# Optimization experiments

Hardware: AMD Instinct MI355X
Metric: run time of the kernel (lower is better)

## Reference

```python
import jax, jax.numpy as jnp
import numpy as np

B = 16          # batch (number of point clouds)
N = 16384       # total points across batch
H = 512         # hidden_size
E = 64          # traj_embed_size
T = 8           # max_traj_len
EB = 72         # euler_bins = 360 // 5
OUT = EB * 3 + 2  # action_mlp output: 216 rot logits + open + stop = 218
TEMP = 1.0


def setup_inputs() -> dict:
    key = jax.random.key(0)
    ks = jax.random.split(key, 8)
    rng = np.random.default_rng(0)
    # ragged segment sizes, each >= 256, summing exactly to N
    counts = rng.multinomial(N - B * 256, np.ones(B) / B) + 256
    s = 0.02
    return {
        "point_embeds": jax.random.normal(ks[0], (N, H), jnp.float32),
        "coords": jax.random.normal(ks[1], (N, 3), jnp.float32),
        "traj_emb": jax.random.normal(ks[2], (T, E), jnp.float32) * s,
        "hm_w1": jax.random.normal(ks[3], (H + E, H), jnp.float32) * s,
        "hm_b1": jnp.zeros((H,), jnp.float32),
        "hm_w2": jax.random.normal(ks[4], (H, 4), jnp.float32) * s,
        "hm_b2": jnp.zeros((4,), jnp.float32),
        "act_w1": jax.random.normal(ks[5], (H + E, H), jnp.float32) * s,
        "act_b1": jnp.zeros((H,), jnp.float32),
        "act_w2": jax.random.normal(ks[6], (H, OUT), jnp.float32) * s,
        "act_b2": jnp.zeros((OUT,), jnp.float32),
        "npoints_in_batch": jnp.asarray(counts, jnp.int32),
    }


def _lrelu(x):
    return jnp.where(x >= 0, x, 0.02 * x)


def reference(point_embeds, coords, traj_emb, hm_w1, hm_b1, hm_w2, hm_b2,
              act_w1, act_b1, act_w2, act_b2, npoints_in_batch):
    n = point_embeds.shape[0]
    # segment id per point (replaces torch.split over ragged batch)
    seg = jnp.repeat(jnp.arange(B), npoints_in_batch, total_repeat_length=n)  # (N,)

    # expand with trajectory-step embedding: (N, T, H+E)
    pe = jnp.concatenate([
        jnp.broadcast_to(point_embeds[:, None, :], (n, T, H)),
        jnp.broadcast_to(traj_emb[None, :, :], (n, T, E)),
    ], axis=-1)

    # heatmap MLP: (N, T, 4) = [heatmap logit, delta xyz]
    hm = _lrelu(pe @ hm_w1 + hm_b1) @ hm_w2 + hm_b2
    logits = hm[..., 0]                                # (N, T)

    # per-segment stable softmax over points
    m = jax.ops.segment_max(logits, seg, num_segments=B)          # (B, T)
    e = jnp.exp((logits - m[seg]) / TEMP)                         # (N, T)
    z = jax.ops.segment_sum(e, seg, num_segments=B)               # (B, T)
    h = e / z[seg]                                                # (N, T)

    new_coords = coords[:, None, :] + hm[..., 1:]                 # (N, T, 3)
    xt = jax.ops.segment_sum(h[..., None] * new_coords, seg, num_segments=B)  # (B, T, 3)

    # reduce == 'max': per-segment max pooling of point embeds
    pc = jax.ops.segment_max(pe, seg, num_segments=B)             # (B, T, H+E)
    ae = _lrelu(pc @ act_w1 + act_b1) @ act_w2 + act_b2           # (B, T, 218)

    xr = ae[..., :EB * 3].reshape(B, T, EB, 3)  # euler_disc logits
    xo = ae[..., -2]
    xstop = ae[..., -1]
    return (xt, xr, xo, xstop)
```

## Files before the change

### kernel.cpp

```cpp
#include <hip/hip_runtime.h>
#include <math.h>

typedef unsigned short u16;
typedef unsigned int u32;

#define NPTS 16384
#define HID  512
#define TT   8
#define TE   64
#define NB   16
#define OUTC 218

typedef short s16x8 __attribute__((ext_vector_type(8)));
typedef float f32x4 __attribute__((ext_vector_type(4)));

__device__ __forceinline__ float bf2f(u16 u) {
  return __uint_as_float(((u32)u) << 16);
}
__device__ __forceinline__ u16 f2bf(float f) {
  u32 x = __float_as_uint(f);
  x += 0x7fffu + ((x >> 16) & 1u);
  return (u16)(x >> 16);
}
__device__ __forceinline__ float lrelu(float h) { return fmaxf(h, 0.02f * h); }

__device__ __forceinline__ float rd(const void* p, size_t i, bool f32) {
  return f32 ? ((const float*)p)[i] : bf2f(((const u16*)p)[i]);
}
__device__ __forceinline__ void wr(void* p, size_t i, bool f32, float v) {
  if (f32) ((float*)p)[i] = v;
  else ((u16*)p)[i] = f2bf(v);
}

__device__ __forceinline__ void split_bf16(float x, u16& hi, u16& lo) {
  const u32 xu = __float_as_uint(x);
  hi = (u16)(xu >> 16);
  const float rem = x - __uint_as_float(xu & 0xffff0000u);
  lo = f2bf(rem);
}

__global__ __launch_bounds__(256) void sniff_kernel(const u16* __restrict__ pe,
                                                    int* __restrict__ flag) {
  __shared__ int s;
  const int tid = threadIdx.x;
  if (tid == 0) s = 0;
  __syncthreads();
  int c = 0;
  for (int i = tid; i < 8192; i += 256) {
    const u16 v = pe[i];
    if ((v & 0x7F80u) == 0x7F80u) c = 1;
  }
  if (c) s = 1;
  __syncthreads();
  if (tid == 0) flag[0] = s;
}

__global__ __launch_bounds__(256) void prep_conv_kernel(
    const void* __restrict__ hm_w1, const void* __restrict__ hm_b1,
    const void* __restrict__ traj, const void* __restrict__ hm_w2,
    const void* __restrict__ hm_b2, const void* __restrict__ aw1,
    const void* __restrict__ ab1, const void* __restrict__ pe,
    const int* __restrict__ npts, float* __restrict__ vprime,
    float* __restrict__ w2f, float* __restrict__ b2f,
    float* __restrict__ avp, u16* __restrict__ Bth, u16* __restrict__ Btl,
    float* __restrict__ partial, const int* __restrict__ flag) {
  const bool f32 = flag[0] != 0;
  const int tid = threadIdx.x, blk = blockIdx.x;
  if (blk < 8) {
    const int t = blk;
    for (int j = tid; j < 512; j += 256) {
      float acc = rd(hm_b1, j, f32);
      for (int e = 0; e < 64; ++e)
        acc = fmaf(rd(traj, t * 64 + e, f32),
                   rd(hm_w1, (size_t)(512 + e) * 512 + j, f32), acc);
      vprime[t * 512 + j] = acc;
    }
  } else if (blk < 16) {
    const int t = blk - 8;
    for (int j = tid; j < 512; j += 256) {
      float acc = rd(ab1, j, f32);
      for (int e = 0; e < 64; ++e)
        acc = fmaf(rd(traj, t * 64 + e, f32),
                   rd(aw1, (size_t)(512 + e) * 512 + j, f32), acc);
      avp[t * 512 + j] = acc;
    }
  } else if (blk == 16) {
    for (int i = tid; i < 2048; i += 256) w2f[i] = rd(hm_w2, i, f32);
    if (tid < 4) b2f[tid] = rd(hm_b2, tid, f32);
  } else if (blk < 145) {
    const int g = (blk - 17) * 256 + tid;
    const int j = g & 511;
    const int kbase = (g >> 9) * 8;
    const int seg = (j >> 4) * 16 + (kbase >> 5);
    const int lane_ = (((kbase >> 3) & 3) << 4) | (j & 15);
    const size_t dst = ((size_t)seg * 64 + lane_) * 8;
    s16x8 hv, lv;
    if (f32) {
      const float* W1 = (const float*)hm_w1;
#pragma unroll
      for (int i = 0; i < 8; ++i) {
        u16 h, l;
        split_bf16(W1[(size_t)(kbase + i) * 512 + j], h, l);
        hv[i] = (short)h;
        lv[i] = (short)l;
      }
      *(s16x8*)&Bth[dst] = hv;
      *(s16x8*)&Btl[dst] = lv;
    } else {
      const u16* W1 = (const u16*)hm_w1;
#pragma unroll
      for (int i = 0; i < 8; ++i) hv[i] = (short)W1[(size_t)(kbase + i) * 512 + j];
      *(s16x8*)&Bth[dst] = hv;
    }
  } else {
    const int blk2 = blk - 145;
    const int b = blk2 >> 4, c = blk2 & 15;
    int s0 = 0, cnt = 0;
    for (int i = 0; i < 16; ++i) {
      const int v = npts[i];
      if (i < b) s0 += v;
      if (i == b) cnt = v;
    }
    const int chunk = (cnt + 15) >> 4;
    const int r0 = s0 + c * chunk;
    int r1 = r0 + chunk;
    const int rend = s0 + cnt;
    if (r1 > rend) r1 = rend;
    const int j2 = tid;
    float m0 = -1e30f, m1 = -1e30f;
    if (f32) {
      const float* pf = (const float*)pe;
      for (int n = r0; n < r1; ++n) {
        const float2 v = *(const float2*)(pf + (size_t)n * 512 + 2 * j2);
        m0 = fmaxf(m0, v.x);
        m1 = fmaxf(m1, v.y);
      }
    } else {
      const u32* p32 = (const u32*)pe;
      for (int n = r0; n < r1; ++n) {
        const u32 v = p32[(size_t)n * 256 + j2];
        m0 = fmaxf(m0, bf2f((u16)(v & 0xffffu)));
        m1 = fmaxf(m1, bf2f((u16)(v >> 16)));
      }
    }
    partial[(size_t)blk2 * 512 + 2 * j2] = m0;
    partial[(size_t)blk2 * 512 + 2 * j2 + 1] = m1;
  }
}

#define SU_STRIDE 516
__global__ __launch_bounds__(1024, 4) void gemm_fused_f32(
    const float* __restrict__ A, const u16* __restrict__ Bth,
    const u16* __restrict__ Btl, const float* __restrict__ vprime,
    const float* __restrict__ w2f, const float* __restrict__ b2f,
    const float* __restrict__ coords, float* __restrict__ logits,
    float* __restrict__ nc, const int* __restrict__ flag) {
  if (flag[0] == 0) return;
  __shared__ __attribute__((aligned(16))) char smem[64 * SU_STRIDE * 4];
  __shared__ float4 sred[512];
  __shared__ float sW2[2048];
  u16* sAh = (u16*)smem;
  u16* sAl = (u16*)(smem + 65536);
  const int tid = threadIdx.x;
  const int rb = blockIdx.x * 64;
  for (int i = tid; i < 2048; i += 1024) sW2[i] = w2f[i];
#pragma unroll
  for (int it = 0; it < 4; ++it) {
    const int c = tid + it * 1024;
    const int row = ((c >> 10) << 4) | (c & 15);
    const int kc = (((c >> 6) & 15) << 2) | ((c >> 4) & 3);
    const float* src = A + (size_t)(rb + row) * 512 + kc * 8;
    const float4 x0 = *(const float4*)(src);
    const float4 x1 = *(const float4*)(src + 4);
    const float xs[8] = {x0.x, x0.y, x0.z, x0.w, x1.x, x1.y, x1.z, x1.w};
    s16x8 hv, lv;
#pragma unroll
    for (int i = 0; i < 8; ++i) {
      u16 h, l;
      split_bf16(xs[i], h, l);
      hv[i] = (short)h;
      lv[i] = (short)l;
    }
    *(s16x8*)&sAh[c * 8] = hv;
    *(s16x8*)&sAl[c * 8] = lv;
  }
  __syncthreads();
  const int wave = tid >> 6, lane = tid & 63;
  f32x4 acc[4][2];
#pragma unroll
  for (int rt = 0; rt < 4; ++rt)
#pragma unroll
    for (int ct = 0; ct < 2; ++ct) acc[rt][ct] = (f32x4){0.f, 0.f, 0.f, 0.f};
  const int bbase = (wave * 2 * 16 * 64 + lane) * 8;
#define LDB(H, L, ks)                                                          \
  {                                                                            \
    H[0] = *(const s16x8*)&Bth[bbase + (ks) * 512];                            \
    H[1] = *(const s16x8*)&Bth[bbase + 8192 + (ks) * 512];                     \
    L[0] = *(const s16x8*)&Btl[bbase + (ks) * 512];                            \
    L[1] = *(const s16x8*)&Btl[bbase + 8192 + (ks) * 512];                     \
  }
#define LDA(ks)                                                                \
  {                                                                            \
    _Pragma("unroll") for (int rt = 0; rt < 4; ++rt) {                         \
      const int aoff = ((rt * 16 + (ks)) * 64 + lane) * 8;                     \
      ah[rt] = *(const s16x8*)&sAh[aoff];                                      \
      al[rt] = *(const s16x8*)&sAl[aoff];                                      \
    }                                                                          \
  }
#define MM(H, L)                                                               \
  _Pragma("unroll") for (int rt = 0; rt < 4; ++rt)                             \
      _Pragma("unroll") for (int ct = 0; ct < 2; ++ct) {                       \
    acc[rt][ct] = __builtin_amdgcn_mfma_f32_16x16x32_bf16(ah[rt], H[ct],       \
                                                          acc[rt][ct], 0, 0,   \
                                                          0);                  \
    acc[rt][ct] = __builtin_amdgcn_mfma_f32_16x16x32_bf16(ah[rt], L[ct],       \
                                                          acc[rt][ct], 0, 0,   \
                                                          0);                  \
    acc[rt][ct] = __builtin_amdgcn_mfma_f32_16x16x32_bf16(al[rt], H[ct],       \
                                                          acc[rt][ct], 0, 0,   \
                                                          0);                  \
  }
  {
    s16x8 ah[4], al[4];
    s16x8 bh0[2], bl0[2], bh1[2], bl1[2];
    LDB(bh0, bl0, 0);
#pragma unroll
    for (int ks = 0; ks < 16; ks += 2) {
      LDB(bh1, bl1, ks + 1);
      LDA(ks);
      MM(bh0, bl0);
      if (ks + 2 < 16) LDB(bh0, bl0, ks + 2);
      LDA(ks + 1);
      MM(bh1, bl1);
    }
  }
#undef LDB
#undef LDA
#undef MM
  __syncthreads();
  float* sU = (float*)smem;
  const int lr = lane & 15, orow = (lane >> 4) * 4;
#pragma unroll
  for (int rt = 0; rt < 4; ++rt)
#pragma unroll
    for (int ct = 0; ct < 2; ++ct) {
      const int col = (wave * 2 + ct) * 16 + lr;
#pragma unroll
      for (int r = 0; r < 4; ++r)
        sU[(rt * 16 + orow + r) * SU_STRIDE + col] = acc[rt][ct][r];
    }
  __syncthreads();
  const int p = tid & 511, half = tid >> 9;
  const int ln = p >> 3, t = p & 7;
  const int n = rb + ln;
  const float* su = sU + ln * SU_STRIDE + half * 256;
  const float* vp = vprime + t * 512 + half * 256;
  const float4* w4 = (const float4*)sW2 + half * 64 * 4;
  float a0 = 0.f, a1 = 0.f, a2 = 0.f, a3 = 0.f;
#pragma unroll 4
  for (int j4 = 0; j4 < 64; ++j4) {
    const float4 uu = *(const float4*)(su + j4 * 4);
    const float4 vv = *(const float4*)(vp + j4 * 4);
    const float4 w_0 = w4[j4 * 4 + 0];
    const float4 w_1 = w4[j4 * 4 + 1];
    const float4 w_2 = w4[j4 * 4 + 2];
    const float4 w_3 = w4[j4 * 4 + 3];
    float h;
    h = lrelu(uu.x + vv.x);
    a0 = fmaf(h, w_0.x, a0); a1 = fmaf(h, w_0.y, a1);
    a2 = fmaf(h, w_0.z, a2); a3 = fmaf(h, w_0.w, a3);
    h = lrelu(uu.y + vv.y);
    a0 = fmaf(h, w_1.x, a0); a1 = fmaf(h, w_1.y, a1);
    a2 = fmaf(h, w_1.z, a2); a3 = fmaf(h, w_1.w, a3);
    h = lrelu(uu.z + vv.z);
    a0 = fmaf(h, w_2.x, a0); a1 = fmaf(h, w_2.y, a1);
    a2 = fmaf(h, w_2.z, a2); a3 = fmaf(h, w_2.w, a3);
    h = lrelu(uu.w + vv.w);
    a0 = fmaf(h, w_3.x, a0); a1 = fmaf(h, w_3.y, a1);
    a2 = fmaf(h, w_3.z, a2); a3 = fmaf(h, w_3.w, a3);
  }
  if (half) sred[p] = make_float4(a0, a1, a2, a3);
  __syncthreads();
  if (!half) {
    const float4 r = sred[p];
    a0 += r.x; a1 += r.y; a2 += r.z; a3 += r.w;
    logits[(size_t)n * 8 + t] = a0 + b2f[0];
    float* o = nc + ((size_t)n * 8 + t) * 3;
    o[0] = coords[(size_t)n * 3 + 0] + a1 + b2f[1];
    o[1] = coords[(size_t)n * 3 + 1] + a2 + b2f[2];
    o[2] = coords[(size_t)n * 3 + 2] + a3 + b2f[3];
  }
}

__global__ __launch_bounds__(1024, 4) void gemm_fused_bf16(
    const u16* __restrict__ A, const u16* __restrict__ Bth,
    const float* __restrict__ vprime, const float* __restrict__ w2f,
    const float* __restrict__ b2f, const u16* __restrict__ coords,
    float* __restrict__ logits, float* __restrict__ nc,
    const int* __restrict__ flag) {
  if (flag[0] != 0) return;
  __shared__ __attribute__((aligned(16))) char smem[64 * SU_STRIDE * 4];
  __shared__ float4 sred[512];
  __shared__ float sW2[2048];
  u16* sAh = (u16*)smem;
  const int tid = threadIdx.x;
  const int rb = blockIdx.x * 64;
  for (int i = tid; i < 2048; i += 1024) sW2[i] = w2f[i];
#pragma unroll
  for (int it = 0; it < 4; ++it) {
    const int c = tid + it * 1024;
    const int row = ((c >> 10) << 4) | (c & 15);
    const int kc = (((c >> 6) & 15) << 2) | ((c >> 4) & 3);
    *(s16x8*)&sAh[c * 8] =
        *(const s16x8*)(A + (size_t)(rb + row) * 512 + kc * 8);
  }
  __syncthreads();
  const int wave = tid >> 6, lane = tid & 63;
  f32x4 acc[4][2];
#pragma unroll
  for (int rt = 0; rt < 4; ++rt)
#pragma unroll
    for (int ct = 0; ct < 2; ++ct) acc[rt][ct] = (f32x4){0.f, 0.f, 0.f, 0.f};
  const int bbase = (wave * 2 * 16 * 64 + lane) * 8;
  {
    s16x8 ah[4], bh[2];
#pragma unroll
    for (int ks = 0; ks < 16; ++ks) {
      bh[0] = *(const s16x8*)&Bth[bbase + ks * 512];
      bh[1] = *(const s16x8*)&Bth[bbase + 8192 + ks * 512];
#pragma unroll
      for (int rt = 0; rt < 4; ++rt)
        ah[rt] = *(const s16x8*)&sAh[((rt * 16 + ks) * 64 + lane) * 8];
#pragma unroll
      for (int rt = 0; rt < 4; ++rt)
#pragma unroll
        for (int ct = 0; ct < 2; ++ct)
          acc[rt][ct] = __builtin_amdgcn_mfma_f32_16x16x32_bf16(
              ah[rt], bh[ct], acc[rt][ct], 0, 0, 0);
    }
  }
  __syncthreads();
  float* sU = (float*)smem;
  const int lr = lane & 15, orow = (lane >> 4) * 4;
#pragma unroll
  for (int rt = 0; rt < 4; ++rt)
#pragma unroll
    for (int ct = 0; ct < 2; ++ct) {
      const int col = (wave * 2 + ct) * 16 + lr;
#pragma unroll
      for (int r = 0; r < 4; ++r)
        sU[(rt * 16 + orow + r) * SU_STRIDE + col] = acc[rt][ct][r];
    }
  __syncthreads();
  const int p = tid & 511, half = tid >> 9;
  const int ln = p >> 3, t = p & 7;
  const int n = rb + ln;
  const float* su = sU + ln * SU_STRIDE + half * 256;
  const float* vp = vprime + t * 512 + half * 256;
  const float4* w4 = (const float4*)sW2 + half * 64 * 4;
  float a0 = 0.f, a1 = 0.f, a2 = 0.f, a3 = 0.f;
#pragma unroll 4
  for (int j4 = 0; j4 < 64; ++j4) {
    const float4 uu = *(const float4*)(su + j4 * 4);
    const float4 vv = *(const float4*)(vp + j4 * 4);
    const float4 w_0 = w4[j4 * 4 + 0];
    const float4 w_1 = w4[j4 * 4 + 1];
    const float4 w_2 = w4[j4 * 4 + 2];
    const float4 w_3 = w4[j4 * 4 + 3];
    float h;
    h = lrelu(uu.x + vv.x);
    a0 = fmaf(h, w_0.x, a0); a1 = fmaf(h, w_0.y, a1);
    a2 = fmaf(h, w_0.z, a2); a3 = fmaf(h, w_0.w, a3);
    h = lrelu(uu.y + vv.y);
    a0 = fmaf(h, w_1.x, a0); a1 = fmaf(h, w_1.y, a1);
    a2 = fmaf(h, w_1.z, a2); a3 = fmaf(h, w_1.w, a3);
    h = lrelu(uu.z + vv.z);
    a0 = fmaf(h, w_2.x, a0); a1 = fmaf(h, w_2.y, a1);
    a2 = fmaf(h, w_2.z, a2); a3 = fmaf(h, w_2.w, a3);
    h = lrelu(uu.w + vv.w);
    a0 = fmaf(h, w_3.x, a0); a1 = fmaf(h, w_3.y, a1);
    a2 = fmaf(h, w_3.z, a2); a3 = fmaf(h, w_3.w, a3);
  }
  if (half) sred[p] = make_float4(a0, a1, a2, a3);
  __syncthreads();
  if (!half) {
    const float4 r = sred[p];
    a0 += r.x; a1 += r.y; a2 += r.z; a3 += r.w;
    logits[(size_t)n * 8 + t] = a0 + b2f[0];
    float* o = nc + ((size_t)n * 8 + t) * 3;
    o[0] = bf2f(coords[(size_t)n * 3 + 0]) + a1 + b2f[1];
    o[1] = bf2f(coords[(size_t)n * 3 + 1]) + a2 + b2f[2];
    o[2] = bf2f(coords[(size_t)n * 3 + 2]) + a3 + b2f[3];
  }
}

__global__ __launch_bounds__(256) void softact_kernel(
    const float* __restrict__ logits, const float* __restrict__ nc,
    const int* __restrict__ npts, const float* __restrict__ partial,
    const void* __restrict__ aw1, const float* __restrict__ avp,
    float* __restrict__ hid, void* __restrict__ out,
    const int* __restrict__ flag) {
  const bool f32 = flag[0] != 0;
  const int tid = threadIdx.x;
  if (blockIdx.x < 128) {
    const int b = blockIdx.x >> 3, t = blockIdx.x & 7;
    int s0 = 0, cnt = 0;
    for (int i = 0; i < 16; ++i) {
      const int v = npts[i];
      if (i < b) s0 += v;
      if (i == b) cnt = v;
    }
    __shared__ float wm[4];
    __shared__ float red[4][4];
    float m = -1e30f;
    for (int i = tid; i < cnt; i += 256)
      m = fmaxf(m, logits[(size_t)(s0 + i) * 8 + t]);
#pragma unroll
    for (int o = 32; o > 0; o >>= 1) m = fmaxf(m, __shfl_down(m, o, 64));
    if ((tid & 63) == 0) wm[tid >> 6] = m;
    __syncthreads();
    const float mt = fmaxf(fmaxf(wm[0], wm[1]), fmaxf(wm[2], wm[3]));
    float z = 0.f, x = 0.f, y = 0.f, w = 0.f;
    for (int i = tid; i < cnt; i += 256) {
      const size_t g = (size_t)(s0 + i) * 8 + t;
      const float e = expf(logits[g] - mt);
      const float* c3 = nc + g * 3;
      z += e;
      x = fmaf(e, c3[0], x);
      y = fmaf(e, c3[1], y);
      w = fmaf(e, c3[2], w);
    }
#pragma unroll
    for (int o = 32; o > 0; o >>= 1) {
      z += __shfl_down(z, o, 64);
      x += __shfl_down(x, o, 64);
      y += __shfl_down(y, o, 64);
      w += __shfl_down(w, o, 64);
    }
    if ((tid & 63) == 0) {
      red[0][tid >> 6] = z; red[1][tid >> 6] = x;
      red[2][tid >> 6] = y; red[3][tid >> 6] = w;
    }
    __syncthreads();
    if (tid == 0) {
      const float Z = red[0][0] + red[0][1] + red[0][2] + red[0][3];
      const float X = red[1][0] + red[1][1] + red[1][2] + red[1][3];
      const float Y = red[2][0] + red[2][1] + red[2][2] + red[2][3];
      const float W = red[3][0] + red[3][1] + red[3][2] + red[3][3];
      wr(out, (size_t)(b * 8 + t) * 3 + 0, f32, X / Z);
      wr(out, (size_t)(b * 8 + t) * 3 + 1, f32, Y / Z);
      wr(out, (size_t)(b * 8 + t) * 3 + 2, f32, W / Z);
    }
  } else {
    const int blk2 = blockIdx.x - 128;
    const int b = blk2 >> 3, jt = blk2 & 7;
    __shared__ float spc[512];
    __shared__ float sred2[4][64];
    for (int k = tid; k < 512; k += 256) {
      float m = -1e30f;
#pragma unroll
      for (int c = 0; c < 16; ++c)
        m = fmaxf(m, partial[(size_t)(b * 16 + c) * 512 + k]);
      spc[k] = m;
    }
    __syncthreads();
    const int jj = tid & 63, kq = tid >> 6;
    const int j = jt * 64 + jj;
    const int kb = kq * 128;
    float a0 = 0.f, a1 = 0.f, a2 = 0.f, a3 = 0.f;
    if (f32) {
      const float* W = (const float*)aw1 + (size_t)kb * 512 + j;
#pragma unroll 4
      for (int k = 0; k < 128; k += 4) {
        a0 = fmaf(spc[kb + k + 0], W[(size_t)(k + 0) * 512], a0);
        a1 = fmaf(spc[kb + k + 1], W[(size_t)(k + 1) * 512], a1);
        a2 = fmaf(spc[kb + k + 2], W[(size_t)(k + 2) * 512], a2);
        a3 = fmaf(spc[kb + k + 3], W[(size_t)(k + 3) * 512], a3);
      }
    } else {
      const u16* W = (const u16*)aw1 + (size_t)kb * 512 + j;
#pragma unroll 4
      for (int k = 0; k < 128; k += 4) {
        a0 = fmaf(spc[kb + k + 0], bf2f(W[(size_t)(k + 0) * 512]), a0);
        a1 = fmaf(spc[kb + k + 1], bf2f(W[(size_t)(k + 1) * 512]), a1);
        a2 = fmaf(spc[kb + k + 2], bf2f(W[(size_t)(k + 2) * 512]), a2);
        a3 = fmaf(spc[kb + k + 3], bf2f(W[(size_t)(k + 3) * 512]), a3);
      }
    }
    sred2[kq][jj] = (a0 + a1) + (a2 + a3);
    __syncthreads();
    if (kq == 0) {
      const float s = (sred2[0][jj] + sred2[1][jj]) + (sred2[2][jj] + sred2[3][jj]);
#pragma unroll
      for (int t = 0; t < 8; ++t)
        hid[(size_t)(b * 8 + t) * 512 + j] = lrelu(s + avp[t * 512 + j]);
    }
  }
}

__global__ __launch_bounds__(256) void act_out_kernel(
    const float* __restrict__ hid, const void* __restrict__ aw2,
    const void* __restrict__ ab2, void* __restrict__ out,
    const int* __restrict__ flag) {
  const bool f32 = flag[0] != 0;
  __shared__ float sh[512];
  const int row = blockIdx.x, tid = threadIdx.x;
  for (int i = tid; i < 512; i += 256) sh[i] = hid[(size_t)row * 512 + i];
  __syncthreads();
  if (tid < OUTC) {
    float a0 = 0.f, a1 = 0.f, a2 = 0.f, a3 = 0.f;
    if (f32) {
      const float* W = (const float*)aw2 + tid;
#pragma unroll 8
      for (int j = 0; j < 512; j += 4) {
        a0 = fmaf(sh[j + 0], W[(size_t)(j + 0) * OUTC], a0);
        a1 = fmaf(sh[j + 1], W[(size_t)(j + 1) * OUTC], a1);
        a2 = fmaf(sh[j + 2], W[(size_t)(j + 2) * OUTC], a2);
        a3 = fmaf(sh[j + 3], W[(size_t)(j + 3) * OUTC], a3);
      }
    } else {
      const u16* W = (const u16*)aw2 + tid;
#pragma unroll 8
      for (int j = 0; j < 512; j += 4) {
        a0 = fmaf(sh[j + 0], bf2f(W[(size_t)(j + 0) * OUTC]), a0);
        a1 = fmaf(sh[j + 1], bf2f(W[(size_t)(j + 1) * OUTC]), a1);
        a2 = fmaf(sh[j + 2], bf2f(W[(size_t)(j + 2) * OUTC]), a2);
        a3 = fmaf(sh[j + 3], bf2f(W[(size_t)(j + 3) * OUTC]), a3);
      }
    }
    const float o = rd(ab2, tid, f32) + ((a0 + a1) + (a2 + a3));
    if (tid < 216)
      wr(out, 384 + (size_t)row * 216 + tid, f32, o);
    else if (tid == 216)
      wr(out, 384 + 27648 + row, f32, o);
    else
      wr(out, 384 + 27648 + 128 + row, f32, o);
  }
}

extern "C" void kernel_launch(void* const* d_in, const int* in_sizes, int n_in,
                              void* d_out, int out_size, void* d_ws,
                              size_t ws_size, hipStream_t stream) {
  (void)in_sizes; (void)n_in; (void)out_size; (void)ws_size;
  const void* pe     = d_in[0];
  const void* coords = d_in[1];
  const void* traj   = d_in[2];
  const void* hm_w1  = d_in[3];
  const void* hm_b1  = d_in[4];
  const void* hm_w2  = d_in[5];
  const void* hm_b2  = d_in[6];
  const void* aw1    = d_in[7];
  const void* ab1    = d_in[8];
  const void* aw2    = d_in[9];
  const void* ab2    = d_in[10];
  const int* npts    = (const int*)d_in[11];

  char* ws = (char*)d_ws;
  int*   flag    = (int*)(ws + 0);
  float* avp     = (float*)(ws + 256);
  float* hid     = (float*)(ws + 16896);
  u16*   Bth     = (u16*)(ws + 524288);
  u16*   Btl     = (u16*)(ws + 1048576);
  float* vprime  = (float*)(ws + 34078720);
  float* w2f     = (float*)(ws + 34095104);
  float* b2f     = (float*)(ws + 34103296);
  float* logits  = (float*)(ws + 34103552);
  float* nc      = (float*)(ws + 34627840);
  float* partial = (float*)(ws + 36200704);

  sniff_kernel<<<1, 256, 0, stream>>>((const u16*)pe, flag);
  prep_conv_kernel<<<401, 256, 0, stream>>>(hm_w1, hm_b1, traj, hm_w2, hm_b2,
                                            aw1, ab1, pe, npts, vprime, w2f,
                                            b2f, avp, Bth, Btl, partial, flag);
  gemm_fused_f32<<<NPTS / 64, 1024, 0, stream>>>((const float*)pe, Bth, Btl,
                                                 vprime, w2f, b2f,
                                                 (const float*)coords, logits,
                                                 nc, flag);
  gemm_fused_bf16<<<NPTS / 64, 1024, 0, stream>>>((const u16*)pe, Bth, vprime,
                                                  w2f, b2f, (const u16*)coords,
                                                  logits, nc, flag);
  softact_kernel<<<256, 256, 0, stream>>>(logits, nc, npts, partial, aw1, avp,
                                          hid, d_out, flag);
  act_out_kernel<<<128, 256, 0, stream>>>(hid, aw2, ab2, d_out, flag);
}
```

Baseline: 183.5 us.

## Double-buffer A and B tiles in LDS via async global_load_lds in fp32 GEMM

The fp32 GEMM path no longer converts the whole 64-row A tile up front or loads B fragments straight from global memory into registers. It now stages one k-slice of A (split into bf16 hi/lo) and B (through global_load_lds) into double-buffered shared memory, overlapping the next slice's loads with the current MFMA work and syncing each step. The W2 copy into shared memory is dropped in both kernels, which now read w2f from global memory. LDS use grows to about 144KB per block, and a barrier is added every k-step.

New measurement: 213.0 us. +16.1%, slower.

```diff
diff --git a/kernel.cpp b/kernel.cpp
--- a/kernel.cpp
+++ b/kernel.cpp
@@ -37,6 +37,12 @@
   hi = (u16)(xu >> 16);
   const float rem = x - __uint_as_float(xu & 0xffff0000u);
   lo = f2bf(rem);
+}
+
+__device__ __forceinline__ void gload16(const void* g, void* l) {
+  __builtin_amdgcn_global_load_lds(
+      (const __attribute__((address_space(1))) unsigned int*)g,
+      (__attribute__((address_space(3))) unsigned int*)l, 16, 0, 0);
 }
 
 __global__ __launch_bounds__(256) void sniff_kernel(const u16* __restrict__ pe,
@@ -149,6 +155,10 @@
 }
 
 #define SU_STRIDE 516
+#define SA_H0 0
+#define SA_L0 8192
+#define SB_H0 16384
+#define SB_L0 81920
 __global__ __launch_bounds__(1024, 4) void gemm_fused_f32(
     const float* __restrict__ A, const u16* __restrict__ Bth,
     const u16* __restrict__ Btl, const float* __restrict__ vprime,
@@ -156,88 +166,80 @@
     const float* __restrict__ coords, float* __restrict__ logits,
     float* __restrict__ nc, const int* __restrict__ flag) {
   if (flag[0] == 0) return;
-  __shared__ __attribute__((aligned(16))) char smem[64 * SU_STRIDE * 4];
+  __shared__ __attribute__((aligned(16))) char smem[147456];
   __shared__ float4 sred[512];
-  __shared__ float sW2[2048];
-  u16* sAh = (u16*)smem;
-  u16* sAl = (u16*)(smem + 65536);
   const int tid = threadIdx.x;
   const int rb = blockIdx.x * 64;
-  for (int i = tid; i < 2048; i += 1024) sW2[i] = w2f[i];
-#pragma unroll
-  for (int it = 0; it < 4; ++it) {
-    const int c = tid + it * 1024;
-    const int row = ((c >> 10) << 4) | (c & 15);
-    const int kc = (((c >> 6) & 15) << 2) | ((c >> 4) & 3);
-    const float* src = A + (size_t)(rb + row) * 512 + kc * 8;
-    const float4 x0 = *(const float4*)(src);
-    const float4 x1 = *(const float4*)(src + 4);
-    const float xs[8] = {x0.x, x0.y, x0.z, x0.w, x1.x, x1.y, x1.z, x1.w};
-    s16x8 hv, lv;
-#pragma unroll
-    for (int i = 0; i < 8; ++i) {
-      u16 h, l;
-      split_bf16(xs[i], h, l);
-      hv[i] = (short)h;
-      lv[i] = (short)l;
-    }
-    *(s16x8*)&sAh[c * 8] = hv;
-    *(s16x8*)&sAl[c * 8] = lv;
-  }
-  __syncthreads();
   const int wave = tid >> 6, lane = tid & 63;
+
+#define STAGE(ks, b)                                                           \
+  {                                                                            \
+    _Pragma("unroll") for (int q = 0; q < 4; ++q) {                            \
+      const int cch = wave * 4 + q;                                            \
+      const int jt2 = cch >> 1;                                                \
+      const u16* gsrc = ((cch & 1) ? Btl : Bth) +                              \
+                        ((size_t)(jt2 * 16 + (ks)) * 64 + lane) * 8;           \
+      char* ldst = smem + ((cch & 1) ? SB_L0 : SB_H0) + (b) * 32768 +          \
+                   jt2 * 1024;                                                 \
+      gload16(gsrc, ldst);                                                     \
+    }                                                                          \
+    const int row_ = tid >> 4, kp_ = tid & 15;                                 \
+    const float2 av = *(const float2*)(A + (size_t)(rb + row_) * 512 +         \
+                                       (ks) * 32 + kp_ * 2);                   \
+    u16 h0, l0, h1, l1;                                                        \
+    split_bf16(av.x, h0, l0);                                                  \
+    split_bf16(av.y, h1, l1);                                                  \
+    const int aoff = (((row_ >> 4) * 64 + ((kp_ >> 2) << 4) + (row_ & 15)) *   \
+                          8 + (kp_ & 3) * 2) * 2;                              \
+    *(u32*)(smem + SA_H0 + (b) * 4096 + aoff) = ((u32)h1 << 16) | h0;          \
+    *(u32*)(smem + SA_L0 + (b) * 4096 + aoff) = ((u32)l1 << 16) | l0;          \
+  }
+
+#define COMPUTE(ks, b)                                                         \
+  {                                                                            \
+    s16x8 ah[4], al[4], bh[2], bl[2];                                          \
+    _Pragma("unroll") for (int ct = 0; ct < 2; ++ct) {                         \
+      const int jt2 = wave * 2 + ct;                                           \
+      bh[ct] = *(const s16x8*)(smem + SB_H0 + (b) * 32768 + jt2 * 1024 +       \
+                               lane * 16);                                     \
+      bl[ct] = *(const s16x8*)(smem + SB_L0 + (b) * 32768 + jt2 * 1024 +       \
+                               lane * 16);                                     \
+    }                                                                          \
+    _Pragma("unroll") for (int rt = 0; rt < 4; ++rt) {                         \
+      ah[rt] = *(const s16x8*)(smem + SA_H0 + (b) * 4096 +                     \
+                               (rt * 64 + lane) * 16);                         \
+      al[rt] = *(const s16x8*)(smem + SA_L0 + (b) * 4096 +                     \
+                               (rt * 64 + lane) * 16);                         \
+    }                                                                          \
+    _Pragma("unroll") for (int rt = 0; rt < 4; ++rt)                           \
+        _Pragma("unroll") for (int ct = 0; ct < 2; ++ct) {                     \
+      acc[rt][ct] = __builtin_amdgcn_mfma_f32_16x16x32_bf16(                   \
+          ah[rt], bh[ct], acc[rt][ct], 0, 0, 0);                               \
+      acc[rt][ct] = __builtin_amdgcn_mfma_f32_16x16x32_bf16(                   \
+          ah[rt], bl[ct], acc[rt][ct], 0, 0, 0);                               \
+      acc[rt][ct] = __builtin_amdgcn_mfma_f32_16x16x32_bf16(                   \
+          al[rt], bh[ct], acc[rt][ct], 0, 0, 0);                               \
+    }                                                                          \
+  }
+
   f32x4 acc[4][2];
 #pragma unroll
   for (int rt = 0; rt < 4; ++rt)
 #pragma unroll
     for (int ct = 0; ct < 2; ++ct) acc[rt][ct] = (f32x4){0.f, 0.f, 0.f, 0.f};
-  const int bbase = (wave * 2 * 16 * 64 + lane) * 8;
-#define LDB(H, L, ks)                                                          \
-  {                                                                            \
-    H[0] = *(const s16x8*)&Bth[bbase + (ks) * 512];                            \
-    H[1] = *(const s16x8*)&Bth[bbase + 8192 + (ks) * 512];                     \
-    L[0] = *(const s16x8*)&Btl[bbase + (ks) * 512];                            \
-    L[1] = *(const s16x8*)&Btl[bbase + 8192 + (ks) * 512];                     \
-  }
-#define LDA(ks)                                                                \
-  {                                                                            \
-    _Pragma("unroll") for (int rt = 0; rt < 4; ++rt) {                         \
-      const int aoff = ((rt * 16 + (ks)) * 64 + lane) * 8;                     \
-      ah[rt] = *(const s16x8*)&sAh[aoff];                                      \
-      al[rt] = *(const s16x8*)&sAl[aoff];                                      \
-    }                                                                          \
-  }
-#define MM(H, L)                                                               \
-  _Pragma("unroll") for (int rt = 0; rt < 4; ++rt)                             \
-      _Pragma("unroll") for (int ct = 0; ct < 2; ++ct) {                       \
-    acc[rt][ct] = __builtin_amdgcn_mfma_f32_16x16x32_bf16(ah[rt], H[ct],       \
-                                                          acc[rt][ct], 0, 0,   \
-                                                          0);                  \
-    acc[rt][ct] = __builtin_amdgcn_mfma_f32_16x16x32_bf16(ah[rt], L[ct],       \
-                                                          acc[rt][ct], 0, 0,   \
-                                                          0);                  \
-    acc[rt][ct] = __builtin_amdgcn_mfma_f32_16x16x32_bf16(al[rt], H[ct],       \
-                                                          acc[rt][ct], 0, 0,   \
-                                                          0);                  \
-  }
-  {
-    s16x8 ah[4], al[4];
-    s16x8 bh0[2], bl0[2], bh1[2], bl1[2];
-    LDB(bh0, bl0, 0);
-#pragma unroll
-    for (int ks = 0; ks < 16; ks += 2) {
-      LDB(bh1, bl1, ks + 1);
-      LDA(ks);
-      MM(bh0, bl0);
-      if (ks + 2 < 16) LDB(bh0, bl0, ks + 2);
-      LDA(ks + 1);
-      MM(bh1, bl1);
-    }
-  }
-#undef LDB
-#undef LDA
-#undef MM
-  __syncthreads();
+
+  STAGE(0, 0);
+  __syncthreads();
+#pragma unroll
+  for (int ks = 0; ks < 16; ++ks) {
+    const int b = ks & 1;
+    if (ks < 15) STAGE(ks + 1, b ^ 1);
+    COMPUTE(ks, b);
+    __syncthreads();
+  }
+#undef STAGE
+#undef COMPUTE
+
   float* sU = (float*)smem;
   const int lr = lane & 15, orow = (lane >> 4) * 4;
 #pragma unroll
@@ -255,7 +257,7 @@
   const int n = rb + ln;
   const float* su = sU + ln * SU_STRIDE + half * 256;
   const float* vp = vprime + t * 512 + half * 256;
-  const float4* w4 = (const float4*)sW2 + half * 64 * 4;
+  const float4* w4 = (const float4*)w2f + half * 256;
   float a0 = 0.f, a1 = 0.f, a2 = 0.f, a3 = 0.f;
 #pragma unroll 4
   for (int j4 = 0; j4 < 64; ++j4) {
@@ -301,11 +303,9 @@
   if (flag[0] != 0) return;
   __shared__ __attribute__((aligned(16))) char smem[64 * SU_STRIDE * 4];
   __shared__ float4 sred[512];
-  __shared__ float sW2[2048];
   u16* sAh = (u16*)smem;
   const int tid = threadIdx.x;
   const int rb = blockIdx.x * 64;
-  for (int i = tid; i < 2048; i += 1024) sW2[i] = w2f[i];
 #pragma unroll
   for (int it = 0; it < 4; ++it) {
     const int c = tid + it * 1024;
@@ -357,7 +357,7 @@
   const int n = rb + ln;
   const float* su = sU + ln * SU_STRIDE + half * 256;
   const float* vp = vprime + t * 512 + half * 256;
-  const float4* w4 = (const float4*)sW2 + half * 64 * 4;
+  const float4* w4 = (const float4*)w2f + half * 256;
   float a0 = 0.f, a1 = 0.f, a2 = 0.f, a3 = 0.f;
 #pragma unroll 4
   for (int j4 = 0; j4 < 64; ++j4) {
```
